# Optimization experiments

Measured on AMD Instinct MI355X. Metric: run time of the kernel, lower is better.

## Reference

```python
import jax, jax.numpy as jnp
import numpy as np

D_MODEL = 512
OUT_MODEL = 512
NUM_HEADS = 8
D_K = OUT_MODEL // NUM_HEADS


def setup_inputs() -> dict:
    key = jax.random.key(0)
    ks = jax.random.split(key, 11)
    B, S = 4, 2048
    inp = {
        "Q": jax.random.normal(ks[0], (B, S, D_MODEL), dtype=jnp.float32),
        "K": jax.random.normal(ks[1], (B, S, D_MODEL), dtype=jnp.float32),
        "V": jax.random.normal(ks[2], (B, S, D_MODEL), dtype=jnp.float32),
    }
    sc = 1.0 / np.sqrt(D_MODEL)
    inp["Wq"] = jax.random.normal(ks[3], (D_MODEL, OUT_MODEL), dtype=jnp.float32) * sc
    inp["bq"] = jnp.zeros((OUT_MODEL,), dtype=jnp.float32)
    inp["Wk"] = jax.random.normal(ks[4], (D_MODEL, OUT_MODEL), dtype=jnp.float32) * sc
    inp["bk"] = jnp.zeros((OUT_MODEL,), dtype=jnp.float32)
    inp["Wv"] = jax.random.normal(ks[5], (D_MODEL, OUT_MODEL), dtype=jnp.float32) * sc
    inp["bv"] = jnp.zeros((OUT_MODEL,), dtype=jnp.float32)
    inp["Wo"] = jax.random.normal(ks[6], (OUT_MODEL, OUT_MODEL), dtype=jnp.float32) * sc
    inp["bo"] = jnp.zeros((OUT_MODEL,), dtype=jnp.float32)
    return inp


def _split_heads(x):
    B, S, _ = x.shape
    return x.reshape(B, S, NUM_HEADS, D_K).transpose(0, 2, 1, 3)  # [B,H,S,Dk]


def reference(Q, K, V, Wq, bq, Wk, bk, Wv, bv, Wo, bo):
    q = _split_heads(Q @ Wq + bq)
    k = _split_heads(K @ Wk + bk)
    v = _split_heads(V @ Wv + bv)
    scores = jnp.einsum("bhsd,bhtd->bhst", q, k) / jnp.sqrt(jnp.float32(D_K))
    probs = jax.nn.softmax(scores, axis=-1)
    attn = jnp.einsum("bhst,bhtd->bhsd", probs, v)  # [B,H,S,Dk]
    B, H, S, Dk = attn.shape
    merged = attn.transpose(0, 2, 1, 3).reshape(B, S, OUT_MODEL)
    return merged @ Wo + bo
```

## Files before the change

### kernel.cpp

```cpp
#include <hip/hip_runtime.h>
#include <hip/hip_bf16.h>
#include <cstdint>


using short8 = __attribute__((ext_vector_type(8))) short;
using f32x4  = __attribute__((ext_vector_type(4))) float;
using f32x16 = __attribute__((ext_vector_type(16))) float;

#define DEVINL __device__ __forceinline__

constexpr int BB  = 4;
constexpr int SS  = 2048;
constexpr int DM  = 512;
constexpr int NH  = 8;
constexpr int DKH = 64;
constexpr float C2 = 0.18033688011112042f;

DEVINL unsigned short f2bf(float f) {
    __hip_bfloat16 h = __float2bfloat16(f);
    return *reinterpret_cast<unsigned short*>(&h);
}

DEVINL f32x4 mfma16(short8 a, short8 b, f32x4 c) {
    return __builtin_amdgcn_mfma_f32_16x16x32_bf16(a, b, c, 0, 0, 0);
}
DEVINL f32x16 mfma32(short8 a, short8 b, f32x16 c) {
    return __builtin_amdgcn_mfma_f32_32x32x16_bf16(a, b, c, 0, 0, 0);
}

DEVINL void gl16(const void* g, void* l) {
    __builtin_amdgcn_global_load_lds(
        (const __attribute__((address_space(1))) unsigned int*)g,
        (__attribute__((address_space(3))) unsigned int*)l, 16, 0, 0);
}
DEVINL void vmcnt0() { asm volatile("s_waitcnt vmcnt(0)" ::: "memory"); }
#define WAIT_VM(N) asm volatile("s_waitcnt vmcnt(" #N ")" ::: "memory")
DEVINL void barrier() { __builtin_amdgcn_s_barrier(); }

DEVINL unsigned cvtpk(float a, float b) {
    unsigned r;
    asm("v_cvt_pk_bf16_f32 %0, %1, %2" : "=v"(r) : "v"(a), "v"(b));
    return r;
}

__global__ __launch_bounds__(256)
void prep_w(const float* __restrict__ Wq, const float* __restrict__ Wk,
            const float* __restrict__ Wv, const float* __restrict__ Wo,
            unsigned short* __restrict__ wt)
{
    const int z = blockIdx.z;
    const float* W = (z == 0) ? Wq : (z == 1) ? Wk : (z == 2) ? Wv : Wo;
    unsigned short* Wtz = wt + (size_t)z * DM * DM;

    __shared__ unsigned short T[64][72];
    const int t = threadIdx.x;
    const int k0 = blockIdx.x * 64, n0 = blockIdx.y * 64;
    const int r = t >> 2, cs = t & 3;

    #pragma unroll
    for (int q = 0; q < 4; ++q) {
        float4 v = *reinterpret_cast<const float4*>(
            &W[(size_t)(k0 + r) * DM + n0 + cs * 16 + q * 4]);
        union { unsigned short u[4]; unsigned long long ll; } pk;
        pk.u[0] = f2bf(v.x); pk.u[1] = f2bf(v.y);
        pk.u[2] = f2bf(v.z); pk.u[3] = f2bf(v.w);
        *reinterpret_cast<unsigned long long*>(&T[r][cs * 16 + q * 4]) = pk.ll;
    }
    __syncthreads();
    union { unsigned short u[8]; short8 v; } p0, p1;
    #pragma unroll
    for (int e = 0; e < 8; ++e) p0.u[e] = T[cs * 16 + e][r];
    #pragma unroll
    for (int e = 0; e < 8; ++e) p1.u[e] = T[cs * 16 + 8 + e][r];
    *reinterpret_cast<short8*>(&Wtz[(size_t)(n0 + r) * DM + k0 + cs * 16]) = p0.v;
    *reinterpret_cast<short8*>(&Wtz[(size_t)(n0 + r) * DM + k0 + cs * 16 + 8]) = p1.v;
}

__global__ __launch_bounds__(256, 4)
void qkv_proj_kernel(const float* __restrict__ Qin, const float* __restrict__ Kin,
                     const float* __restrict__ Vin,
                     const unsigned short* __restrict__ wt,
                     const float* __restrict__ bq, const float* __restrict__ bk,
                     const float* __restrict__ bv,
                     unsigned short* __restrict__ qb, unsigned short* __restrict__ kb,
                     unsigned short* __restrict__ vt)
{
    const int z = blockIdx.z;
    const float* A           = (z == 0) ? Qin : (z == 1) ? Kin : Vin;
    const unsigned short* Wt = wt + (size_t)z * DM * DM;
    const float* bias        = (z == 0) ? bq : (z == 1) ? bk : bv;

    __shared__ unsigned short As[2][128][32];
    __shared__ unsigned short Bs[2][128][32];

    const int tid = threadIdx.x, lane = tid & 63, w = tid >> 6;
    const int wm = w >> 1, wn = w & 1;
    const int row16 = lane & 15, kg = lane >> 4;
    const int m0tok = blockIdx.x * 128, n0ch = blockIdx.y * 128;

    const int ar = tid >> 1, ah = tid & 1;

    float4 apf[4];
    auto load_A = [&](int kt) {
        const float* Ap = &A[(size_t)(m0tok + ar) * DM + kt * 32 + ah * 16];
        #pragma unroll
        for (int q = 0; q < 4; ++q)
            apf[q] = *reinterpret_cast<const float4*>(Ap + q * 4);
    };
    auto write_A = [&](int buf) {
        #pragma unroll
        for (int s = 0; s < 2; ++s) {
            union { unsigned short u[8]; short8 v; } pk;
            float4 a = apf[2 * s], b = apf[2 * s + 1];
            pk.u[0] = f2bf(a.x); pk.u[1] = f2bf(a.y);
            pk.u[2] = f2bf(a.z); pk.u[3] = f2bf(a.w);
            pk.u[4] = f2bf(b.x); pk.u[5] = f2bf(b.y);
            pk.u[6] = f2bf(b.z); pk.u[7] = f2bf(b.w);
            int phys = (ah * 2 + s) ^ (ar & 3);
            *reinterpret_cast<short8*>(&As[buf][ar][phys * 8]) = pk.v;
        }
    };
    auto issue_B = [&](int kt, int buf) {
        #pragma unroll
        for (int i = 0; i < 2; ++i) {
            int chunk = tid + i * 256;
            int n = chunk >> 2, c = chunk & 3;
            const unsigned short* src =
                &Wt[(size_t)(n0ch + n) * DM + kt * 32 + ((c ^ (n & 3)) * 8)];
            gl16(src, (char*)&Bs[buf][0][0] + (size_t)(w * 64 + i * 256) * 16);
        }
    };

    f32x4 acc[4][4] = {};
    const int aoff = ((z == 2) ? wn : wm) * 64;
    const int boff = ((z == 2) ? wm : wn) * 64;

    load_A(0); issue_B(0, 0);
    vmcnt0();
    write_A(0);
    __syncthreads();

    for (int t = 0; t < 16; ++t) {
        const int cur = t & 1, nxt = cur ^ 1;
        if (t + 1 < 16) { issue_B(t + 1, nxt); load_A(t + 1); }

        short8 af[4], bfr[4];
        #pragma unroll
        for (int i = 0; i < 4; ++i) {
            int ra = aoff + i * 16 + row16;
            int rb = boff + i * 16 + row16;
            af[i]  = *reinterpret_cast<const short8*>(
                &As[cur][ra][((kg ^ (ra & 3)) * 8)]);
            bfr[i] = *reinterpret_cast<const short8*>(
                &Bs[cur][rb][((kg ^ (rb & 3)) * 8)]);
        }
        __builtin_amdgcn_s_setprio(1);
        #pragma unroll
        for (int mf = 0; mf < 4; ++mf)
            #pragma unroll
            for (int nf = 0; nf < 4; ++nf)
                acc[mf][nf] = (z == 2)
                    ? mfma16(bfr[mf], af[nf], acc[mf][nf])
                    : mfma16(af[mf], bfr[nf], acc[mf][nf]);
        __builtin_amdgcn_s_setprio(0);

        vmcnt0();
        if (t + 1 < 16) write_A(nxt);
        __syncthreads();
    }

    if (z < 2) {
        unsigned short* C = (z == 0) ? qb : kb;
        const float osc = (z == 0) ? C2 : 1.0f;
        #pragma unroll
        for (int nf = 0; nf < 4; ++nf) {
            int ch = n0ch + wn * 64 + nf * 16 + row16;
            float bval = bias[ch];
            int h = ch >> 6, dk = ch & 63;
            #pragma unroll
            for (int mf = 0; mf < 4; ++mf)
                #pragma unroll
                for (int j = 0; j < 4; ++j) {
                    int tok = m0tok + wm * 64 + mf * 16 + kg * 4 + j;
                    int b = tok >> 11, s = tok & 2047;
                    C[(((size_t)b * NH + h) * SS + s) * DKH + dk] =
                        f2bf((acc[mf][nf][j] + bval) * osc);
                }
        }
    } else {
        #pragma unroll
        for (int mf = 0; mf < 4; ++mf)
            #pragma unroll
            for (int j = 0; j < 4; ++j) {
                int ch = n0ch + wm * 64 + mf * 16 + kg * 4 + j;
                float bval = bias[ch];
                int h = ch >> 6, dk = ch & 63;
                #pragma unroll
                for (int nf = 0; nf < 4; ++nf) {
                    int tok = m0tok + wn * 64 + nf * 16 + row16;
                    int b = tok >> 11, s = tok & 2047;
                    vt[(((size_t)b * NH + h) * DKH + dk) * SS + s] =
                        f2bf(acc[mf][nf][j] + bval);
                }
            }
    }
}

__global__ __launch_bounds__(256, 2)
void attn_kernel(const unsigned short* __restrict__ qb,
                 const unsigned short* __restrict__ kb,
                 const unsigned short* __restrict__ vt,
                 unsigned short* __restrict__ am)
{
    __shared__ unsigned short Qs[128][64];
    __shared__ unsigned short Ks[3][64 * 64];
    __shared__ unsigned short Vs[3][64 * 64];

    const int tid = threadIdx.x, lane = tid & 63, w = tid >> 6;
    const int l31 = lane & 31, hi = lane >> 5;
    const int bh = blockIdx.y, b = bh >> 3, h = bh & 7;
    const int q0 = blockIdx.x * 128;
    const size_t base = (size_t)bh * SS * DKH;

    auto stage_KV = [&](int t0, int buf) {
        #pragma unroll
        for (int i = 0; i < 2; ++i) {
            int cc = tid + i * 256;
            int r = cc >> 3, c = cc & 7;
            gl16(&kb[base + (size_t)(t0 + r) * DKH + ((c ^ (r & 7)) * 8)],
                 (char*)Ks + (size_t)buf * 8192 + (size_t)(w * 64 + i * 256) * 16);
            gl16(&vt[base + (size_t)r * SS + t0 + ((c ^ (r & 7)) * 8)],
                 (char*)Vs + (size_t)buf * 8192 + (size_t)(w * 64 + i * 256) * 16);
        }
    };

    #pragma unroll
    for (int i = 0; i < 4; ++i) {
        int cc = tid + i * 256;
        int r = cc >> 3, c = cc & 7;
        gl16(&qb[base + (size_t)(q0 + r) * DKH + ((c ^ (r & 7)) * 8)],
             (char*)&Qs[0][0] + (size_t)(w * 64 + i * 256) * 16);
    }
    stage_KV(0, 0);
    stage_KV(64, 1);
    WAIT_VM(4);
    barrier();

    short8 qf[4];
    const int qrow = w * 32 + l31;
    #pragma unroll
    for (int ks = 0; ks < 4; ++ks) {
        int c = ks * 2 + hi;
        qf[ks] = *reinterpret_cast<const short8*>(
            &Qs[qrow][((c ^ (qrow & 7)) * 8)]);
    }

    f32x16 o[2] = {};
    float lsum = 0.f;

    for (int tt = 0; tt < 32; ++tt) {
        const int cur = tt % 3;
        if (tt + 2 < 32) stage_KV((tt + 2) * 64, (tt + 2) % 3);

        f32x16 sfr[2] = {};
        __builtin_amdgcn_s_setprio(1);
        #pragma unroll
        for (int ks = 0; ks < 4; ++ks)
            #pragma unroll
            for (int mkv = 0; mkv < 2; ++mkv) {
                int row = mkv * 32 + l31;
                int c = ks * 2 + hi;
                short8 kf = *reinterpret_cast<const short8*>(
                    &Ks[cur][row * 64 + ((c ^ (row & 7)) * 8)]);
                sfr[mkv] = mfma32(kf, qf[ks], sfr[mkv]);
            }
        __builtin_amdgcn_s_setprio(0);

        unsigned pk[2][4][2];
        #pragma unroll
        for (int mkv = 0; mkv < 2; ++mkv)
            #pragma unroll
            for (int bq = 0; bq < 4; ++bq) {
                float p0 = __builtin_amdgcn_exp2f(sfr[mkv][bq * 4 + 0]);
                float p1 = __builtin_amdgcn_exp2f(sfr[mkv][bq * 4 + 1]);
                float p2 = __builtin_amdgcn_exp2f(sfr[mkv][bq * 4 + 2]);
                float p3 = __builtin_amdgcn_exp2f(sfr[mkv][bq * 4 + 3]);
                lsum += (p0 + p1) + (p2 + p3);
                pk[mkv][bq][0] = cvtpk(p0, p1);
                pk[mkv][bq][1] = cvtpk(p2, p3);
            }

        __builtin_amdgcn_s_setprio(1);
        #pragma unroll
        for (int ks2 = 0; ks2 < 4; ++ks2) {
            const int mkv = ks2 >> 1, b0 = (ks2 & 1) * 2, b1 = b0 + 1;
            unsigned x0 = pk[mkv][b0][0], y0 = pk[mkv][b1][0];
            unsigned x1 = pk[mkv][b0][1], y1 = pk[mkv][b1][1];
            asm volatile("v_permlane32_swap_b32 %0, %1" : "+v"(x0), "+v"(y0));
            asm volatile("v_permlane32_swap_b32 %0, %1" : "+v"(x1), "+v"(y1));
            union { unsigned u[4]; short8 s; } pa;
            pa.u[0] = x0; pa.u[1] = x1; pa.u[2] = y0; pa.u[3] = y1;
            #pragma unroll
            for (int ndk = 0; ndk < 2; ++ndk) {
                int row = ndk * 32 + l31;
                int c = ks2 * 2 + hi;
                short8 vf = *reinterpret_cast<const short8*>(
                    &Vs[cur][row * 64 + ((c ^ (row & 7)) * 8)]);
                o[ndk] = mfma32(pa.s, vf, o[ndk]);
            }
        }
        __builtin_amdgcn_s_setprio(0);

        if (tt + 2 < 32)      { WAIT_VM(4); }
        else if (tt + 1 < 32) { WAIT_VM(0); }
        if (tt + 1 < 32) barrier();
    }

    float lfull = lsum + __shfl_xor(lsum, 32, 64);
    float linv = 1.0f / lfull;
    #pragma unroll
    for (int r = 0; r < 16; ++r) {
        int qloc = (r & 3) + 8 * (r >> 2) + 4 * hi;
        float li = __shfl(linv, qloc, 64);
        int sg = q0 + w * 32 + qloc;
        #pragma unroll
        for (int ndk = 0; ndk < 2; ++ndk) {
            int dk = ndk * 32 + l31;
            am[((size_t)b * SS + sg) * DM + h * DKH + dk] =
                f2bf(o[ndk][r] * li);
        }
    }
}

__global__ __launch_bounds__(256, 4)
void out_proj_kernel(const unsigned short* __restrict__ am,
                     const unsigned short* __restrict__ Wt,
                     const float* __restrict__ bo,
                     float* __restrict__ out)
{
    __shared__ unsigned short As[2][64 * 32];
    __shared__ unsigned short Bs[2][128 * 32];

    const int tid = threadIdx.x, lane = tid & 63, w = tid >> 6;
    const int wm = w & 1, wn = w >> 1;
    const int row16 = lane & 15, kg = lane >> 4;
    const int m0 = blockIdx.x * 64;
    const int n0 = blockIdx.y * 128;

    auto stage = [&](int kt, int buf) {
        {
            int r = tid >> 2, c = tid & 3;
            gl16(&am[(size_t)(m0 + r) * DM + kt * 32 + ((c ^ (r & 3)) * 8)],
                 (char*)As + (size_t)buf * 4096 + (size_t)(w * 64) * 16);
        }
        #pragma unroll
        for (int i = 0; i < 2; ++i) {
            int cc = tid + i * 256;
            int n = cc >> 2, c = cc & 3;
            gl16(&Wt[(size_t)(n0 + n) * DM + kt * 32 + ((c ^ (n & 3)) * 8)],
                 (char*)Bs + (size_t)buf * 8192 + (size_t)(w * 64 + i * 256) * 16);
        }
    };

    f32x4 acc[2][4] = {};

    stage(0, 0);
    vmcnt0();
    __syncthreads();

    for (int t = 0; t < 16; ++t) {
        const int cur = t & 1, nxt = cur ^ 1;
        if (t + 1 < 16) stage(t + 1, nxt);

        short8 af[2], bfr[4];
        #pragma unroll
        for (int i = 0; i < 2; ++i) {
            int ra = wm * 32 + i * 16 + row16;
            af[i] = *reinterpret_cast<const short8*>(
                &As[cur][ra * 32 + ((kg ^ (ra & 3)) * 8)]);
        }
        #pragma unroll
        for (int i = 0; i < 4; ++i) {
            int rb = wn * 64 + i * 16 + row16;
            bfr[i] = *reinterpret_cast<const short8*>(
                &Bs[cur][rb * 32 + ((kg ^ (rb & 3)) * 8)]);
        }
        __builtin_amdgcn_s_setprio(1);
        #pragma unroll
        for (int mf = 0; mf < 2; ++mf)
            #pragma unroll
            for (int nf = 0; nf < 4; ++nf)
                acc[mf][nf] = mfma16(af[mf], bfr[nf], acc[mf][nf]);
        __builtin_amdgcn_s_setprio(0);

        vmcnt0();
        __syncthreads();
    }

    #pragma unroll
    for (int nf = 0; nf < 4; ++nf) {
        int n = n0 + wn * 64 + nf * 16 + row16;
        float bval = bo[n];
        #pragma unroll
        for (int mf = 0; mf < 2; ++mf)
            #pragma unroll
            for (int j = 0; j < 4; ++j) {
                int mrow = m0 + wm * 32 + mf * 16 + kg * 4 + j;
                out[(size_t)mrow * DM + n] = acc[mf][nf][j] + bval;
            }
    }
}

extern "C" void kernel_launch(void* const* d_in, const int* in_sizes, int n_in,
                              void* d_out, int out_size, void* d_ws, size_t ws_size,
                              hipStream_t stream) {
    const float* Q  = (const float*)d_in[0];
    const float* K  = (const float*)d_in[1];
    const float* V  = (const float*)d_in[2];
    const float* Wq = (const float*)d_in[3];
    const float* bq = (const float*)d_in[4];
    const float* Wk = (const float*)d_in[5];
    const float* bk = (const float*)d_in[6];
    const float* Wv = (const float*)d_in[7];
    const float* bv = (const float*)d_in[8];
    const float* Wo = (const float*)d_in[9];
    const float* bo = (const float*)d_in[10];
    float* out = (float*)d_out;

    const size_t per = (size_t)BB * NH * SS * DKH;
    unsigned short* qb = (unsigned short*)d_ws;
    unsigned short* kb = qb + per;
    unsigned short* vt = kb + per;
    unsigned short* am = vt + per;
    unsigned short* wt = am + per;

    prep_w<<<dim3(8, 8, 4), 256, 0, stream>>>(Wq, Wk, Wv, Wo, wt);
    qkv_proj_kernel<<<dim3(64, 4, 3), 256, 0, stream>>>(
        Q, K, V, wt, bq, bk, bv, qb, kb, vt);
    attn_kernel<<<dim3(SS / 128, BB * NH), 256, 0, stream>>>(qb, kb, vt, am);
    out_proj_kernel<<<dim3(128, 4), 256, 0, stream>>>(
        am, wt + 3 * (size_t)DM * DM, bo, out);
}
```

Baseline: 94.11 us.

## Pre-tile K/V layout and give each attention wave two query tiles

The QKV projection now writes K and V in a pre-tiled order that matches the LDS fragment reads. Staging becomes contiguous 16-byte copies and the XOR swizzle is gone. Each attention block now handles 256 queries, each wave 64 queries split into two 32-row tiles, so every K and V fragment read from LDS feeds two MFMAs. This halves LDS traffic per unit of compute, and Q fragments are loaded straight from global memory. In exchange the grid is halved, launch bounds drop to one block per CU and register pressure rises, which reduces occupancy and latency hiding.

```diff
diff --git a/kernel.cpp b/kernel.cpp
--- a/kernel.cpp
+++ b/kernel.cpp
@@ -82,8 +82,8 @@
                      const unsigned short* __restrict__ wt,
                      const float* __restrict__ bq, const float* __restrict__ bk,
                      const float* __restrict__ bv,
-                     unsigned short* __restrict__ qb, unsigned short* __restrict__ kb,
-                     unsigned short* __restrict__ vt)
+                     unsigned short* __restrict__ qb, unsigned short* __restrict__ kb2,
+                     unsigned short* __restrict__ vt2)
 {
     const int z = blockIdx.z;
     const float* A           = (z == 0) ? Qin : (z == 1) ? Kin : Vin;
@@ -170,7 +170,6 @@
     }
 
     if (z < 2) {
-        unsigned short* C = (z == 0) ? qb : kb;
         const float osc = (z == 0) ? C2 : 1.0f;
         #pragma unroll
         for (int nf = 0; nf < 4; ++nf) {
@@ -183,8 +182,14 @@
                 for (int j = 0; j < 4; ++j) {
                     int tok = m0tok + wm * 64 + mf * 16 + kg * 4 + j;
                     int b = tok >> 11, s = tok & 2047;
-                    C[(((size_t)b * NH + h) * SS + s) * DKH + dk] =
-                        f2bf((acc[mf][nf][j] + bval) * osc);
+                    float val = (acc[mf][nf][j] + bval) * osc;
+                    if (z == 0) {
+                        qb[(((size_t)b * NH + h) * SS + s) * DKH + dk] = f2bf(val);
+                    } else {
+                        kb2[(size_t)(b * NH + h) * (SS * DKH) +
+                            (size_t)(s >> 6) * 4096 + (dk >> 3) * 512 +
+                            (s & 63) * 8 + (dk & 7)] = f2bf(val);
+                    }
                 }
         }
     } else {
@@ -199,114 +204,115 @@
                 for (int nf = 0; nf < 4; ++nf) {
                     int tok = m0tok + wn * 64 + nf * 16 + row16;
                     int b = tok >> 11, s = tok & 2047;
-                    vt[(((size_t)b * NH + h) * DKH + dk) * SS + s] =
+                    vt2[(size_t)(b * NH + h) * (SS * DKH) +
+                        (size_t)(s >> 3) * 512 + dk * 8 + (s & 7)] =
                         f2bf(acc[mf][nf][j] + bval);
                 }
             }
     }
 }
 
-__global__ __launch_bounds__(256, 2)
+__global__ __launch_bounds__(256, 1)
 void attn_kernel(const unsigned short* __restrict__ qb,
-                 const unsigned short* __restrict__ kb,
-                 const unsigned short* __restrict__ vt,
+                 const unsigned short* __restrict__ kb2,
+                 const unsigned short* __restrict__ vt2,
                  unsigned short* __restrict__ am)
 {
-    __shared__ unsigned short Qs[128][64];
-    __shared__ unsigned short Ks[3][64 * 64];
-    __shared__ unsigned short Vs[3][64 * 64];
+    __shared__ unsigned short Ks[3][4096];
+    __shared__ unsigned short Vs[3][4096];
 
     const int tid = threadIdx.x, lane = tid & 63, w = tid >> 6;
     const int l31 = lane & 31, hi = lane >> 5;
     const int bh = blockIdx.y, b = bh >> 3, h = bh & 7;
-    const int q0 = blockIdx.x * 128;
-    const size_t base = (size_t)bh * SS * DKH;
-
-    auto stage_KV = [&](int t0, int buf) {
+    const int q0 = blockIdx.x * 256;
+    const size_t base = (size_t)bh * (SS * DKH);
+
+    auto stage_KV = [&](int tt, int buf) {
+        const unsigned short* ksrc = kb2 + base + (size_t)tt * 4096;
+        const unsigned short* vsrc = vt2 + base + (size_t)tt * 4096;
         #pragma unroll
         for (int i = 0; i < 2; ++i) {
-            int cc = tid + i * 256;
-            int r = cc >> 3, c = cc & 7;
-            gl16(&kb[base + (size_t)(t0 + r) * DKH + ((c ^ (r & 7)) * 8)],
-                 (char*)Ks + (size_t)buf * 8192 + (size_t)(w * 64 + i * 256) * 16);
-            gl16(&vt[base + (size_t)r * SS + t0 + ((c ^ (r & 7)) * 8)],
-                 (char*)Vs + (size_t)buf * 8192 + (size_t)(w * 64 + i * 256) * 16);
+            int cb = i * 256 + w * 64;
+            gl16(ksrc + (size_t)(cb + lane) * 8, (char*)Ks[buf] + (size_t)cb * 16);
+            gl16(vsrc + (size_t)(cb + lane) * 8, (char*)Vs[buf] + (size_t)cb * 16);
         }
     };
 
-    #pragma unroll
-    for (int i = 0; i < 4; ++i) {
-        int cc = tid + i * 256;
-        int r = cc >> 3, c = cc & 7;
-        gl16(&qb[base + (size_t)(q0 + r) * DKH + ((c ^ (r & 7)) * 8)],
-             (char*)&Qs[0][0] + (size_t)(w * 64 + i * 256) * 16);
-    }
+    short8 qf[2][4];
+    #pragma unroll
+    for (int tq = 0; tq < 2; ++tq) {
+        int qrow = q0 + w * 64 + tq * 32 + l31;
+        #pragma unroll
+        for (int ks = 0; ks < 4; ++ks)
+            qf[tq][ks] = *reinterpret_cast<const short8*>(
+                &qb[base + (size_t)qrow * DKH + (ks * 2 + hi) * 8]);
+    }
+    vmcnt0();
+
     stage_KV(0, 0);
-    stage_KV(64, 1);
+    stage_KV(1, 1);
     WAIT_VM(4);
     barrier();
 
-    short8 qf[4];
-    const int qrow = w * 32 + l31;
-    #pragma unroll
-    for (int ks = 0; ks < 4; ++ks) {
-        int c = ks * 2 + hi;
-        qf[ks] = *reinterpret_cast<const short8*>(
-            &Qs[qrow][((c ^ (qrow & 7)) * 8)]);
-    }
-
-    f32x16 o[2] = {};
-    float lsum = 0.f;
+    f32x16 o[2][2] = {};
+    float lsum[2] = {0.f, 0.f};
 
     for (int tt = 0; tt < 32; ++tt) {
         const int cur = tt % 3;
-        if (tt + 2 < 32) stage_KV((tt + 2) * 64, (tt + 2) % 3);
-
-        f32x16 sfr[2] = {};
+        if (tt + 2 < 32) stage_KV(tt + 2, (tt + 2) % 3);
+
+        f32x16 sfr[2][2] = {};
         __builtin_amdgcn_s_setprio(1);
         #pragma unroll
-        for (int ks = 0; ks < 4; ++ks)
+        for (int ks = 0; ks < 4; ++ks) {
+            int c = ks * 2 + hi;
             #pragma unroll
             for (int mkv = 0; mkv < 2; ++mkv) {
-                int row = mkv * 32 + l31;
-                int c = ks * 2 + hi;
                 short8 kf = *reinterpret_cast<const short8*>(
-                    &Ks[cur][row * 64 + ((c ^ (row & 7)) * 8)]);
-                sfr[mkv] = mfma32(kf, qf[ks], sfr[mkv]);
-            }
+                    &Ks[cur][(c * 64 + mkv * 32 + l31) * 8]);
+                sfr[0][mkv] = mfma32(kf, qf[0][ks], sfr[0][mkv]);
+                sfr[1][mkv] = mfma32(kf, qf[1][ks], sfr[1][mkv]);
+            }
+        }
         __builtin_amdgcn_s_setprio(0);
 
-        unsigned pk[2][4][2];
-        #pragma unroll
-        for (int mkv = 0; mkv < 2; ++mkv)
-            #pragma unroll
-            for (int bq = 0; bq < 4; ++bq) {
-                float p0 = __builtin_amdgcn_exp2f(sfr[mkv][bq * 4 + 0]);
-                float p1 = __builtin_amdgcn_exp2f(sfr[mkv][bq * 4 + 1]);
-                float p2 = __builtin_amdgcn_exp2f(sfr[mkv][bq * 4 + 2]);
-                float p3 = __builtin_amdgcn_exp2f(sfr[mkv][bq * 4 + 3]);
-                lsum += (p0 + p1) + (p2 + p3);
-                pk[mkv][bq][0] = cvtpk(p0, p1);
-                pk[mkv][bq][1] = cvtpk(p2, p3);
-            }
+        unsigned pk[2][2][4][2];
+        #pragma unroll
+        for (int tq = 0; tq < 2; ++tq)
+            #pragma unroll
+            for (int mkv = 0; mkv < 2; ++mkv)
+                #pragma unroll
+                for (int bq = 0; bq < 4; ++bq) {
+                    float p0 = __builtin_amdgcn_exp2f(sfr[tq][mkv][bq * 4 + 0]);
+                    float p1 = __builtin_amdgcn_exp2f(sfr[tq][mkv][bq * 4 + 1]);
+                    float p2 = __builtin_amdgcn_exp2f(sfr[tq][mkv][bq * 4 + 2]);
+                    float p3 = __builtin_amdgcn_exp2f(sfr[tq][mkv][bq * 4 + 3]);
+                    lsum[tq] += (p0 + p1) + (p2 + p3);
+                    pk[tq][mkv][bq][0] = cvtpk(p0, p1);
+                    pk[tq][mkv][bq][1] = cvtpk(p2, p3);
+                }
 
         __builtin_amdgcn_s_setprio(1);
         #pragma unroll
         for (int ks2 = 0; ks2 < 4; ++ks2) {
             const int mkv = ks2 >> 1, b0 = (ks2 & 1) * 2, b1 = b0 + 1;
-            unsigned x0 = pk[mkv][b0][0], y0 = pk[mkv][b1][0];
-            unsigned x1 = pk[mkv][b0][1], y1 = pk[mkv][b1][1];
-            asm volatile("v_permlane32_swap_b32 %0, %1" : "+v"(x0), "+v"(y0));
-            asm volatile("v_permlane32_swap_b32 %0, %1" : "+v"(x1), "+v"(y1));
-            union { unsigned u[4]; short8 s; } pa;
-            pa.u[0] = x0; pa.u[1] = x1; pa.u[2] = y0; pa.u[3] = y1;
+            union { unsigned u[4]; short8 s; } pa[2];
+            #pragma unroll
+            for (int tq = 0; tq < 2; ++tq) {
+                unsigned x0 = pk[tq][mkv][b0][0], y0 = pk[tq][mkv][b1][0];
+                unsigned x1 = pk[tq][mkv][b0][1], y1 = pk[tq][mkv][b1][1];
+                asm volatile("v_permlane32_swap_b32 %0, %1" : "+v"(x0), "+v"(y0));
+                asm volatile("v_permlane32_swap_b32 %0, %1" : "+v"(x1), "+v"(y1));
+                pa[tq].u[0] = x0; pa[tq].u[1] = x1;
+                pa[tq].u[2] = y0; pa[tq].u[3] = y1;
+            }
+            int c = ks2 * 2 + hi;
             #pragma unroll
             for (int ndk = 0; ndk < 2; ++ndk) {
-                int row = ndk * 32 + l31;
-                int c = ks2 * 2 + hi;
                 short8 vf = *reinterpret_cast<const short8*>(
-                    &Vs[cur][row * 64 + ((c ^ (row & 7)) * 8)]);
-                o[ndk] = mfma32(pa.s, vf, o[ndk]);
+                    &Vs[cur][(c * 64 + ndk * 32 + l31) * 8]);
+                o[0][ndk] = mfma32(pa[0].s, vf, o[0][ndk]);
+                o[1][ndk] = mfma32(pa[1].s, vf, o[1][ndk]);
             }
         }
         __builtin_amdgcn_s_setprio(0);
@@ -316,18 +322,21 @@
         if (tt + 1 < 32) barrier();
     }
 
-    float lfull = lsum + __shfl_xor(lsum, 32, 64);
-    float linv = 1.0f / lfull;
-    #pragma unroll
-    for (int r = 0; r < 16; ++r) {
-        int qloc = (r & 3) + 8 * (r >> 2) + 4 * hi;
-        float li = __shfl(linv, qloc, 64);
-        int sg = q0 + w * 32 + qloc;
-        #pragma unroll
-        for (int ndk = 0; ndk < 2; ++ndk) {
-            int dk = ndk * 32 + l31;
-            am[((size_t)b * SS + sg) * DM + h * DKH + dk] =
-                f2bf(o[ndk][r] * li);
+    #pragma unroll
+    for (int tq = 0; tq < 2; ++tq) {
+        float lfull = lsum[tq] + __shfl_xor(lsum[tq], 32, 64);
+        float linv = 1.0f / lfull;
+        #pragma unroll
+        for (int r = 0; r < 16; ++r) {
+            int qloc = (r & 3) + 8 * (r >> 2) + 4 * hi;
+            float li = __shfl(linv, qloc, 64);
+            int sg = q0 + w * 64 + tq * 32 + qloc;
+            #pragma unroll
+            for (int ndk = 0; ndk < 2; ++ndk) {
+                int dk = ndk * 32 + l31;
+                am[((size_t)b * SS + sg) * DM + h * DKH + dk] =
+                    f2bf(o[tq][ndk][r] * li);
+            }
         }
     }
 }
@@ -428,16 +437,16 @@
     float* out = (float*)d_out;
 
     const size_t per = (size_t)BB * NH * SS * DKH;
-    unsigned short* qb = (unsigned short*)d_ws;
-    unsigned short* kb = qb + per;
-    unsigned short* vt = kb + per;
-    unsigned short* am = vt + per;
-    unsigned short* wt = am + per;
+    unsigned short* qb  = (unsigned short*)d_ws;
+    unsigned short* kb2 = qb + per;
+    unsigned short* vt2 = kb2 + per;
+    unsigned short* am  = vt2 + per;
+    unsigned short* wt  = am + per;
 
     prep_w<<<dim3(8, 8, 4), 256, 0, stream>>>(Wq, Wk, Wv, Wo, wt);
     qkv_proj_kernel<<<dim3(64, 4, 3), 256, 0, stream>>>(
-        Q, K, V, wt, bq, bk, bv, qb, kb, vt);
-    attn_kernel<<<dim3(SS / 128, BB * NH), 256, 0, stream>>>(qb, kb, vt, am);
+        Q, K, V, wt, bq, bk, bv, qb, kb2, vt2);
+    attn_kernel<<<dim3(SS / 256, BB * NH), 256, 0, stream>>>(qb, kb2, vt2, am);
     out_proj_kernel<<<dim3(128, 4), 256, 0, stream>>>(
         am, wt + 3 * (size_t)DM * DM, bo, out);
 }
```

Result: slower. 110.5 us (+17.5%).
